# Kernel optimization log

Hardware: AMD Instinct MI355X
Metric: run time of the kernel (lower is better)

## Reference

```python
import jax, jax.numpy as jnp
import numpy as np

FILTS = 100  # conv padding = aconv_filts
SCALING = 2.0


def setup_inputs() -> dict:
    key = jax.random.key(0)
    ks = jax.random.split(key, 9)
    T, DUNITS, ATT, EPROJ, CH, K = 50000, 1024, 512, 512, 10, 2 * FILTS + 1
    return {
        "dec_z": jax.random.normal(ks[0], (1, DUNITS), jnp.float32),
        "att_prev": jax.random.uniform(ks[1], (1, T), jnp.float32),
        "pre_compute_enc_h": jax.random.normal(ks[2], (1, T, ATT), jnp.float32),
        "enc_h": jax.random.normal(ks[3], (1, T, EPROJ), jnp.float32),
        "mask": jnp.zeros((1, T), jnp.float32),
        "conv_w": jax.random.normal(ks[4], (CH, 1, K), jnp.float32) * 0.05,
        "w_att": jax.random.normal(ks[5], (ATT, CH), jnp.float32) * 0.05,
        "w_dec": jax.random.normal(ks[6], (ATT, DUNITS), jnp.float32) * 0.02,
        "w_gvec": jax.random.normal(ks[7], (1, ATT), jnp.float32) * 0.05,
        "b_gvec": jnp.zeros((1,), jnp.float32),
    }


def reference(dec_z, att_prev, pre_compute_enc_h, enc_h, mask, conv_w, w_att, w_dec, w_gvec, b_gvec):
    # loc_conv: 1-channel 1D conv over previous attention weights -> [1, CH, T]
    att_conv = jax.lax.conv_general_dilated(
        att_prev[:, None, :], conv_w, window_strides=(1,),
        padding=[(FILTS, FILTS)], dimension_numbers=("NCH", "OIH", "NCH"))
    # mlp_att: [1, T, ATT]
    att_conv = jnp.einsum("bct,ac->bta", att_conv, w_att)
    # mlp_dec, tiled over frames: [1, 1, ATT]
    dec_tiled = (dec_z @ w_dec.T)[:, None, :]
    # gvec(tanh(...)) -> scores e: [1, T]
    e = jnp.einsum("bta,a->bt", jnp.tanh(att_conv + pre_compute_enc_h + dec_tiled), w_gvec[0]) + b_gvec
    e = e + mask
    w = jax.nn.softmax(SCALING * e, axis=1)  # [1, T]
    c = jnp.sum(enc_h * w[..., None], axis=1)  # [1, EPROJ]
    return (c, w)
```

## Files before the change

### kernel.cpp

```cpp
#include <hip/hip_runtime.h>
#include <math.h>


constexpr int ATT    = 512;
constexpr int CH     = 10;
constexpr int PCH    = 12;
constexpr int KW     = 201;
constexpr int FILTS  = 100;
constexpr int DUNITS = 1024;
constexpr int NB1    = 1024;
constexpr int NB3    = 1024;
constexpr int CT     = 64;
constexpr float SCALING = 2.0f;

__device__ __forceinline__ float wave_reduce_sum(float v) {
    #pragma unroll
    for (int off = 32; off > 0; off >>= 1) v += __shfl_xor(v, off, 64);
    return v;
}

__device__ __forceinline__ float fast_tanh(float x) {
    float e = __expf(2.f * x);
    return 1.f - __fdividef(2.f, e + 1.f);
}

__global__ __launch_bounds__(256, 4) void k0_conv_dec(
    const float* __restrict__ att_prev,
    const float* __restrict__ conv_w,
    const float* __restrict__ dec_z,
    const float* __restrict__ w_dec,
    float* __restrict__ ws_aconv,
    float* __restrict__ ws_dec,
    float* __restrict__ out,
    int T, int nbconv)
{
    if ((int)blockIdx.x < nbconv) {
        __shared__ float s_ap[CT + KW - 1];
        __shared__ float s_wt[KW * 12];
        __shared__ float s_part[4 * CT * CH];
        const int t0 = blockIdx.x * CT;
        for (int i = threadIdx.x; i < CT + KW - 1; i += 256) {
            int t = t0 - FILTS + i;
            s_ap[i] = (t >= 0 && t < T) ? att_prev[t] : 0.f;
        }
        for (int i = threadIdx.x; i < CH * KW; i += 256) {
            int c = i % CH, k = i / CH;
            s_wt[k * 12 + c] = conv_w[c * KW + k];
        }
        __syncthreads();
        const int tl = threadIdx.x & 63;
        const int kq = threadIdx.x >> 6;
        float acc[CH];
        #pragma unroll
        for (int c = 0; c < CH; ++c) acc[c] = 0.f;
        for (int k = kq; k < KW; k += 4) {
            float x = s_ap[tl + k];
            const float4 w0 = *(const float4*)&s_wt[k * 12];
            const float4 w1 = *(const float4*)&s_wt[k * 12 + 4];
            const float2 w2 = *(const float2*)&s_wt[k * 12 + 8];
            acc[0] += x * w0.x; acc[1] += x * w0.y;
            acc[2] += x * w0.z; acc[3] += x * w0.w;
            acc[4] += x * w1.x; acc[5] += x * w1.y;
            acc[6] += x * w1.z; acc[7] += x * w1.w;
            acc[8] += x * w2.x; acc[9] += x * w2.y;
        }
        #pragma unroll
        for (int c = 0; c < CH; ++c) s_part[kq * (CT * CH) + tl * CH + c] = acc[c];
        __syncthreads();
        for (int idx = threadIdx.x; idx < CT * PCH; idx += 256) {
            int t = idx / PCH, c = idx % PCH;
            float v = 0.f;
            if (c < CH) {
                int j = t * CH + c;
                v = s_part[j] + s_part[CT * CH + j]
                  + s_part[2 * CT * CH + j] + s_part[3 * CT * CH + j];
            }
            if (t0 + t < T) ws_aconv[(size_t)(t0 + t) * PCH + c] = v;
        }
    } else {
        const int b    = blockIdx.x - nbconv;
        const int wid  = threadIdx.x >> 6;
        const int lane = threadIdx.x & 63;
        const int a    = b * 4 + wid;
        if (threadIdx.x < 4) out[b * 4 + threadIdx.x] = 0.f;
        const float4* wd = (const float4*)(w_dec + (size_t)a * DUNITS);
        const float4* dz = (const float4*)dec_z;
        float acc = 0.f;
        #pragma unroll
        for (int q = 0; q < 4; ++q) {
            float4 wv = wd[lane + q * 64];
            float4 zv = dz[lane + q * 64];
            acc += wv.x * zv.x + wv.y * zv.y + wv.z * zv.z + wv.w * zv.w;
        }
        acc = wave_reduce_sum(acc);
        if (lane == 0) ws_dec[a] = acc;
    }
}

__global__ __launch_bounds__(256, 2) void k1_scores(
    const float* __restrict__ pre,
    const float* __restrict__ mask,
    const float* __restrict__ w_att,
    const float* __restrict__ w_gvec,
    const float* __restrict__ b_gvec,
    const float* __restrict__ ws_dec,
    const float* __restrict__ ws_aconv,
    float* __restrict__ ws_e,
    float* __restrict__ ws_ms,
    int T)
{
    __shared__ float s_m[4], s_s[4];
    const int wid  = threadIdx.x >> 6;
    const int lane = threadIdx.x & 63;

    float wa[8][CH];
    #pragma unroll
    for (int j = 0; j < 4; ++j) {
        #pragma unroll
        for (int c = 0; c < CH; ++c) {
            wa[j][c]     = w_att[(lane * 4 + j) * CH + c];
            wa[4 + j][c] = w_att[(256 + lane * 4 + j) * CH + c];
        }
    }
    const float4 dlo = ((const float4*)ws_dec)[lane];
    const float4 dhi = ((const float4*)ws_dec)[64 + lane];
    const float4 glo = ((const float4*)w_gvec)[lane];
    const float4 ghi = ((const float4*)w_gvec)[64 + lane];
    const float  bg  = b_gvec[0];

    const float4* pre4 = (const float4*)pre;
    const float4* ac4  = (const float4*)ws_aconv;
    const int gw = blockIdx.x * 4 + wid;
    const int t0 = gw * 4;
    constexpr int S = NB1 * 16;

    float m = -INFINITY, s = 0.f;
    float4 pA0[4], pA1[4], pB0[4], pB1[4];
    float  mA[4], mB[4];
    float4 acx[4], acy[4], acz[4];

    auto loadp = [&](float4 (&P0)[4], float4 (&P1)[4], float (&MSK)[4], int tb) {
        #pragma unroll
        for (int i = 0; i < 4; ++i) {
            int t = tb + i;
            if (t < T) {
                P0[i]  = pre4[(size_t)t * 128 + lane];
                P1[i]  = pre4[(size_t)t * 128 + 64 + lane];
                MSK[i] = mask[t];
            }
        }
    };
    auto loada = [&](int tb) {
        #pragma unroll
        for (int i = 0; i < 4; ++i) {
            int t = tb + i;
            if (t < T) {
                acx[i] = ac4[(size_t)t * 3 + 0];
                acy[i] = ac4[(size_t)t * 3 + 1];
                acz[i] = ac4[(size_t)t * 3 + 2];
            }
        }
    };
    auto batch = [&](float4 (&P0)[4], float4 (&P1)[4], float (&MSK)[4], int tb,
                     float4 (&NP0)[4], float4 (&NP1)[4], float (&NM)[4], int tn,
                     bool pf) {
        if (pf) loadp(NP0, NP1, NM, tn);
        float y[4];
        #pragma unroll
        for (int i = 0; i < 4; ++i) {
            const int t = tb + i;
            y[i] = -INFINITY;
            if (t < T) {
                const float4 a0 = acx[i], a1 = acy[i], a2 = acz[i];
                float x0 = P0[i].x + dlo.x, x1 = P0[i].y + dlo.y;
                float x2 = P0[i].z + dlo.z, x3 = P0[i].w + dlo.w;
                float x4 = P1[i].x + dhi.x, x5 = P1[i].y + dhi.y;
                float x6 = P1[i].z + dhi.z, x7 = P1[i].w + dhi.w;
                #define AV(X, J) \
                    X += a0.x*wa[J][0] + a0.y*wa[J][1] + a0.z*wa[J][2] + a0.w*wa[J][3] \
                       + a1.x*wa[J][4] + a1.y*wa[J][5] + a1.z*wa[J][6] + a1.w*wa[J][7] \
                       + a2.x*wa[J][8] + a2.y*wa[J][9]
                AV(x0, 0); AV(x1, 1); AV(x2, 2); AV(x3, 3);
                AV(x4, 4); AV(x5, 5); AV(x6, 6); AV(x7, 7);
                #undef AV
                float acc = glo.x * fast_tanh(x0) + glo.y * fast_tanh(x1)
                          + glo.z * fast_tanh(x2) + glo.w * fast_tanh(x3)
                          + ghi.x * fast_tanh(x4) + ghi.y * fast_tanh(x5)
                          + ghi.z * fast_tanh(x6) + ghi.w * fast_tanh(x7);
                acc = wave_reduce_sum(acc);
                float yy = SCALING * (acc + bg + MSK[i]);
                if (lane == 0) ws_e[t] = yy;
                y[i] = yy;
            }
        }
        if (pf) loada(tn);
        float ymax = fmaxf(fmaxf(y[0], y[1]), fmaxf(y[2], y[3]));
        float nm = fmaxf(m, ymax);
        float add = __expf(y[0] - nm) + __expf(y[1] - nm)
                  + __expf(y[2] - nm) + __expf(y[3] - nm);
        s = s * __expf(m - nm) + add;
        m = nm;
    };

    loadp(pA0, pA1, mA, t0);
    loada(t0);
    batch(pA0, pA1, mA, t0,         pB0, pB1, mB, t0 + S,     true);
    batch(pB0, pB1, mB, t0 + S,     pA0, pA1, mA, t0 + 2 * S, true);
    batch(pA0, pA1, mA, t0 + 2 * S, pB0, pB1, mB, t0 + 3 * S, true);
    batch(pB0, pB1, mB, t0 + 3 * S, pA0, pA1, mA, 0,          false);

    if (lane == 0) { s_m[wid] = m; s_s[wid] = s; }
    __syncthreads();
    if (threadIdx.x == 0) {
        float M = s_m[0], Ssum = s_s[0];
        #pragma unroll
        for (int w = 1; w < 4; ++w) {
            float m2 = s_m[w], s2 = s_s[w];
            float nm = fmaxf(M, m2);
            Ssum = Ssum * __expf(M - nm) + s2 * __expf(m2 - nm);
            M = nm;
        }
        ws_ms[blockIdx.x * 2]     = M;
        ws_ms[blockIdx.x * 2 + 1] = Ssum;
    }
}

__global__ __launch_bounds__(256, 4) void k3_ctx(
    const float* __restrict__ enc_h,
    const float* __restrict__ ws_e,
    const float* __restrict__ ws_ms,
    float* __restrict__ out,
    int T)
{
    __shared__ float s_m[256], s_s[256];
    {
        float m = -INFINITY, s = 0.f;
        for (int i = threadIdx.x; i < NB1; i += 256) {
            float m2 = ws_ms[i * 2], s2 = ws_ms[i * 2 + 1];
            float nm = fmaxf(m, m2);
            s = s * __expf(m - nm) + s2 * __expf(m2 - nm);
            m = nm;
        }
        s_m[threadIdx.x] = m; s_s[threadIdx.x] = s;
        __syncthreads();
        for (int off = 128; off > 0; off >>= 1) {
            if ((int)threadIdx.x < off) {
                float M1 = s_m[threadIdx.x], S1 = s_s[threadIdx.x];
                float m2 = s_m[threadIdx.x + off], s2 = s_s[threadIdx.x + off];
                float nm = fmaxf(M1, m2);
                s_s[threadIdx.x] = S1 * __expf(M1 - nm) + s2 * __expf(m2 - nm);
                s_m[threadIdx.x] = nm;
            }
            __syncthreads();
        }
    }
    const float M  = s_m[0];
    const float IS = 1.f / s_s[0];

    const int wid  = threadIdx.x >> 6;
    const int lane = threadIdx.x & 63;
    const float4* eh4 = (const float4*)enc_h;
    const int gw = blockIdx.x * 4 + wid;
    const int t0 = gw * 4;
    constexpr int S = NB3 * 16;

    float4 a0 = make_float4(0.f, 0.f, 0.f, 0.f);
    float4 a1 = make_float4(0.f, 0.f, 0.f, 0.f);
    float4 eA0[4], eA1[4], eB0[4], eB1[4];
    float  yA[4], yB[4];

    auto loade = [&](float4 (&E0)[4], float4 (&E1)[4], float (&Y)[4], int tb) {
        #pragma unroll
        for (int i = 0; i < 4; ++i) {
            int t = tb + i;
            if (t < T) {
                E0[i] = eh4[(size_t)t * 128 + lane];
                E1[i] = eh4[(size_t)t * 128 + 64 + lane];
                Y[i]  = ws_e[t];
            }
        }
    };
    auto batch = [&](float4 (&E0)[4], float4 (&E1)[4], float (&Y)[4], int tb,
                     float4 (&NE0)[4], float4 (&NE1)[4], float (&NY)[4], int tn,
                     bool pf) {
        if (pf) loade(NE0, NE1, NY, tn);
        #pragma unroll
        for (int i = 0; i < 4; ++i) {
            int t = tb + i;
            if (t < T) {
                float w = __expf(Y[i] - M) * IS;
                if (lane == 0) out[ATT + t] = w;
                a0.x += w * E0[i].x; a0.y += w * E0[i].y;
                a0.z += w * E0[i].z; a0.w += w * E0[i].w;
                a1.x += w * E1[i].x; a1.y += w * E1[i].y;
                a1.z += w * E1[i].z; a1.w += w * E1[i].w;
            }
        }
    };

    loade(eA0, eA1, yA, t0);
    batch(eA0, eA1, yA, t0,         eB0, eB1, yB, t0 + S,     true);
    batch(eB0, eB1, yB, t0 + S,     eA0, eA1, yA, t0 + 2 * S, true);
    batch(eA0, eA1, yA, t0 + 2 * S, eB0, eB1, yB, t0 + 3 * S, true);
    batch(eB0, eB1, yB, t0 + 3 * S, eA0, eA1, yA, 0,          false);

    __syncthreads();
    __shared__ float4 s_c[4 * 128];
    s_c[wid * 128 + lane]      = a0;
    s_c[wid * 128 + 64 + lane] = a1;
    __syncthreads();
    const float* sc = (const float*)s_c;
    for (int a = threadIdx.x; a < ATT; a += 256) {
        float v = sc[a] + sc[512 + a] + sc[1024 + a] + sc[1536 + a];
        atomicAdd(&out[a], v);
    }
}

extern "C" void kernel_launch(void* const* d_in, const int* in_sizes, int n_in,
                              void* d_out, int out_size, void* d_ws, size_t ws_size,
                              hipStream_t stream)
{
    const float* dec_z    = (const float*)d_in[0];
    const float* att_prev = (const float*)d_in[1];
    const float* pre      = (const float*)d_in[2];
    const float* enc_h    = (const float*)d_in[3];
    const float* mask     = (const float*)d_in[4];
    const float* conv_w   = (const float*)d_in[5];
    const float* w_att    = (const float*)d_in[6];
    const float* w_dec    = (const float*)d_in[7];
    const float* w_gvec   = (const float*)d_in[8];
    const float* b_gvec   = (const float*)d_in[9];
    const int T = in_sizes[1];

    float* ws       = (float*)d_ws;
    float* ws_dec   = ws;
    float* ws_aconv = ws_dec + ATT;
    float* ws_e     = ws_aconv + (size_t)T * PCH;
    float* ws_ms    = ws_e + T;
    float* out      = (float*)d_out;

    const int nbconv = (T + CT - 1) / CT;

    hipLaunchKernelGGL(k0_conv_dec, dim3(nbconv + ATT / 4), dim3(256), 0, stream,
                       att_prev, conv_w, dec_z, w_dec, ws_aconv, ws_dec, out, T, nbconv);
    hipLaunchKernelGGL(k1_scores, dim3(NB1), dim3(256), 0, stream,
                       pre, mask, w_att, w_gvec, b_gvec, ws_dec, ws_aconv,
                       ws_e, ws_ms, T);
    hipLaunchKernelGGL(k3_ctx, dim3(NB3), dim3(256), 0, stream,
                       enc_h, ws_e, ws_ms, out, T);
}
```

Measured before the change: 299.0 us.

## Fuse context accumulation into score kernel with online-softmax rescaling

```diff
diff --git a/kernel.cpp b/kernel.cpp
--- a/kernel.cpp
+++ b/kernel.cpp
@@ -9,7 +9,6 @@
 constexpr int FILTS  = 100;
 constexpr int DUNITS = 1024;
 constexpr int NB1    = 1024;
-constexpr int NB3    = 1024;
 constexpr int CT     = 64;
 constexpr float SCALING = 2.0f;
 
@@ -31,7 +30,6 @@
     const float* __restrict__ w_dec,
     float* __restrict__ ws_aconv,
     float* __restrict__ ws_dec,
-    float* __restrict__ out,
     int T, int nbconv)
 {
     if ((int)blockIdx.x < nbconv) {
@@ -82,7 +80,6 @@
         const int wid  = threadIdx.x >> 6;
         const int lane = threadIdx.x & 63;
         const int a    = b * 4 + wid;
-        if (threadIdx.x < 4) out[b * 4 + threadIdx.x] = 0.f;
         const float4* wd = (const float4*)(w_dec + (size_t)a * DUNITS);
         const float4* dz = (const float4*)dec_z;
         float acc = 0.f;
@@ -97,8 +94,9 @@
     }
 }
 
-__global__ __launch_bounds__(256, 2) void k1_scores(
+__global__ __launch_bounds__(256, 3) void k1_scores(
     const float* __restrict__ pre,
+    const float* __restrict__ enc_h,
     const float* __restrict__ mask,
     const float* __restrict__ w_att,
     const float* __restrict__ w_gvec,
@@ -107,9 +105,9 @@
     const float* __restrict__ ws_aconv,
     float* __restrict__ ws_e,
     float* __restrict__ ws_ms,
+    float* __restrict__ ws_c,
     int T)
 {
-    __shared__ float s_m[4], s_s[4];
     const int wid  = threadIdx.x >> 6;
     const int lane = threadIdx.x & 63;
 
@@ -129,12 +127,15 @@
     const float  bg  = b_gvec[0];
 
     const float4* pre4 = (const float4*)pre;
+    const float4* eh4  = (const float4*)enc_h;
     const float4* ac4  = (const float4*)ws_aconv;
     const int gw = blockIdx.x * 4 + wid;
     const int t0 = gw * 4;
     constexpr int S = NB1 * 16;
 
     float m = -INFINITY, s = 0.f;
+    float4 cA0 = make_float4(0.f, 0.f, 0.f, 0.f);
+    float4 cA1 = make_float4(0.f, 0.f, 0.f, 0.f);
     float4 pA0[4], pA1[4], pB0[4], pB1[4];
     float  mA[4], mB[4];
     float4 acx[4], acy[4], acz[4];
@@ -165,6 +166,17 @@
                      float4 (&NP0)[4], float4 (&NP1)[4], float (&NM)[4], int tn,
                      bool pf) {
         if (pf) loadp(NP0, NP1, NM, tn);
+        float4 E0[4], E1[4];
+        const float4 z4 = make_float4(0.f, 0.f, 0.f, 0.f);
+        #pragma unroll
+        for (int i = 0; i < 4; ++i) {
+            int t = tb + i;
+            E0[i] = z4; E1[i] = z4;
+            if (t < T) {
+                E0[i] = eh4[(size_t)t * 128 + lane];
+                E1[i] = eh4[(size_t)t * 128 + 64 + lane];
+            }
+        }
         float y[4];
         #pragma unroll
         for (int i = 0; i < 4; ++i) {
@@ -196,9 +208,18 @@
         if (pf) loada(tn);
         float ymax = fmaxf(fmaxf(y[0], y[1]), fmaxf(y[2], y[3]));
         float nm = fmaxf(m, ymax);
-        float add = __expf(y[0] - nm) + __expf(y[1] - nm)
-                  + __expf(y[2] - nm) + __expf(y[3] - nm);
-        s = s * __expf(m - nm) + add;
+        float sc = __expf(m - nm);
+        float w0 = __expf(y[0] - nm), w1 = __expf(y[1] - nm);
+        float w2 = __expf(y[2] - nm), w3 = __expf(y[3] - nm);
+        s = s * sc + (w0 + w1 + w2 + w3);
+        cA0.x = cA0.x * sc + w0*E0[0].x + w1*E0[1].x + w2*E0[2].x + w3*E0[3].x;
+        cA0.y = cA0.y * sc + w0*E0[0].y + w1*E0[1].y + w2*E0[2].y + w3*E0[3].y;
+        cA0.z = cA0.z * sc + w0*E0[0].z + w1*E0[1].z + w2*E0[2].z + w3*E0[3].z;
+        cA0.w = cA0.w * sc + w0*E0[0].w + w1*E0[1].w + w2*E0[2].w + w3*E0[3].w;
+        cA1.x = cA1.x * sc + w0*E1[0].x + w1*E1[1].x + w2*E1[2].x + w3*E1[3].x;
+        cA1.y = cA1.y * sc + w0*E1[0].y + w1*E1[1].y + w2*E1[2].y + w3*E1[3].y;
+        cA1.z = cA1.z * sc + w0*E1[0].z + w1*E1[1].z + w2*E1[2].z + w3*E1[3].z;
+        cA1.w = cA1.w * sc + w0*E1[0].w + w1*E1[1].w + w2*E1[2].w + w3*E1[3].w;
         m = nm;
     };
 
@@ -209,26 +230,32 @@
     batch(pA0, pA1, mA, t0 + 2 * S, pB0, pB1, mB, t0 + 3 * S, true);
     batch(pB0, pB1, mB, t0 + 3 * S, pA0, pA1, mA, 0,          false);
 
-    if (lane == 0) { s_m[wid] = m; s_s[wid] = s; }
+    __shared__ float4 s_c[4 * 128];
+    __shared__ float  s_mw[4], s_sw[4];
+    s_c[wid * 128 + lane]      = cA0;
+    s_c[wid * 128 + 64 + lane] = cA1;
+    if (lane == 0) { s_mw[wid] = m; s_sw[wid] = s; }
     __syncthreads();
+    const float mb = fmaxf(fmaxf(s_mw[0], s_mw[1]), fmaxf(s_mw[2], s_mw[3]));
+    const float sc0 = __expf(s_mw[0] - mb), sc1 = __expf(s_mw[1] - mb);
+    const float sc2 = __expf(s_mw[2] - mb), sc3 = __expf(s_mw[3] - mb);
+    const float* scf = (const float*)s_c;
+    for (int a = threadIdx.x; a < ATT; a += 256) {
+        float v = sc0 * scf[a] + sc1 * scf[512 + a]
+                + sc2 * scf[1024 + a] + sc3 * scf[1536 + a];
+        ws_c[(size_t)blockIdx.x * ATT + a] = v;
+    }
     if (threadIdx.x == 0) {
-        float M = s_m[0], Ssum = s_s[0];
-        #pragma unroll
-        for (int w = 1; w < 4; ++w) {
-            float m2 = s_m[w], s2 = s_s[w];
-            float nm = fmaxf(M, m2);
-            Ssum = Ssum * __expf(M - nm) + s2 * __expf(m2 - nm);
-            M = nm;
-        }
-        ws_ms[blockIdx.x * 2]     = M;
-        ws_ms[blockIdx.x * 2 + 1] = Ssum;
-    }
-}
-
-__global__ __launch_bounds__(256, 4) void k3_ctx(
-    const float* __restrict__ enc_h,
+        ws_ms[blockIdx.x * 2]     = mb;
+        ws_ms[blockIdx.x * 2 + 1] = sc0 * s_sw[0] + sc1 * s_sw[1]
+                                  + sc2 * s_sw[2] + sc3 * s_sw[3];
+    }
+}
+
+__global__ __launch_bounds__(256, 4) void k2_final(
     const float* __restrict__ ws_e,
     const float* __restrict__ ws_ms,
+    const float* __restrict__ ws_c,
     float* __restrict__ out,
     int T)
 {
@@ -257,63 +284,30 @@
     const float M  = s_m[0];
     const float IS = 1.f / s_s[0];
 
-    const int wid  = threadIdx.x >> 6;
-    const int lane = threadIdx.x & 63;
-    const float4* eh4 = (const float4*)enc_h;
-    const int gw = blockIdx.x * 4 + wid;
-    const int t0 = gw * 4;
-    constexpr int S = NB3 * 16;
-
-    float4 a0 = make_float4(0.f, 0.f, 0.f, 0.f);
-    float4 a1 = make_float4(0.f, 0.f, 0.f, 0.f);
-    float4 eA0[4], eA1[4], eB0[4], eB1[4];
-    float  yA[4], yB[4];
-
-    auto loade = [&](float4 (&E0)[4], float4 (&E1)[4], float (&Y)[4], int tb) {
-        #pragma unroll
-        for (int i = 0; i < 4; ++i) {
-            int t = tb + i;
-            if (t < T) {
-                E0[i] = eh4[(size_t)t * 128 + lane];
-                E1[i] = eh4[(size_t)t * 128 + 64 + lane];
-                Y[i]  = ws_e[t];
-            }
-        }
-    };
-    auto batch = [&](float4 (&E0)[4], float4 (&E1)[4], float (&Y)[4], int tb,
-                     float4 (&NE0)[4], float4 (&NE1)[4], float (&NY)[4], int tn,
-                     bool pf) {
-        if (pf) loade(NE0, NE1, NY, tn);
-        #pragma unroll
-        for (int i = 0; i < 4; ++i) {
-            int t = tb + i;
-            if (t < T) {
-                float w = __expf(Y[i] - M) * IS;
-                if (lane == 0) out[ATT + t] = w;
-                a0.x += w * E0[i].x; a0.y += w * E0[i].y;
-                a0.z += w * E0[i].z; a0.w += w * E0[i].w;
-                a1.x += w * E1[i].x; a1.y += w * E1[i].y;
-                a1.z += w * E1[i].z; a1.w += w * E1[i].w;
-            }
-        }
-    };
-
-    loade(eA0, eA1, yA, t0);
-    batch(eA0, eA1, yA, t0,         eB0, eB1, yB, t0 + S,     true);
-    batch(eB0, eB1, yB, t0 + S,     eA0, eA1, yA, t0 + 2 * S, true);
-    batch(eA0, eA1, yA, t0 + 2 * S, eB0, eB1, yB, t0 + 3 * S, true);
-    batch(eB0, eB1, yB, t0 + 3 * S, eA0, eA1, yA, 0,          false);
-
-    __syncthreads();
-    __shared__ float4 s_c[4 * 128];
-    s_c[wid * 128 + lane]      = a0;
-    s_c[wid * 128 + 64 + lane] = a1;
-    __syncthreads();
-    const float* sc = (const float*)s_c;
-    for (int a = threadIdx.x; a < ATT; a += 256) {
-        float v = sc[a] + sc[512 + a] + sc[1024 + a] + sc[1536 + a];
-        atomicAdd(&out[a], v);
-    }
+    if (blockIdx.x < 32) {
+        __shared__ float s_scale[NB1];
+        for (int b = threadIdx.x; b < NB1; b += 256)
+            s_scale[b] = __expf(ws_ms[b * 2] - M);
+        __syncthreads();
+        const int al = threadIdx.x >> 4;
+        const int ch = threadIdx.x & 15;
+        const int a  = blockIdx.x * 16 + al;
+        float acc = 0.f;
+        for (int b = ch * (NB1 / 16); b < (ch + 1) * (NB1 / 16); ++b)
+            acc += s_scale[b] * ws_c[(size_t)b * ATT + a];
+        __shared__ float s_p[256];
+        s_p[threadIdx.x] = acc;
+        __syncthreads();
+        if (ch == 0) {
+            float v = 0.f;
+            #pragma unroll
+            for (int k = 0; k < 16; ++k) v += s_p[al * 16 + k];
+            out[a] = v * IS;
+        }
+    }
+
+    const int t = blockIdx.x * 256 + threadIdx.x;
+    if (t < T) out[ATT + t] = __expf(ws_e[t] - M) * IS;
 }
 
 extern "C" void kernel_launch(void* const* d_in, const int* in_sizes, int n_in,
@@ -337,15 +331,17 @@
     float* ws_aconv = ws_dec + ATT;
     float* ws_e     = ws_aconv + (size_t)T * PCH;
     float* ws_ms    = ws_e + T;
+    float* ws_c     = ws_ms + NB1 * 2;
     float* out      = (float*)d_out;
 
     const int nbconv = (T + CT - 1) / CT;
+    const int nb2    = (T + 255) / 256;
 
     hipLaunchKernelGGL(k0_conv_dec, dim3(nbconv + ATT / 4), dim3(256), 0, stream,
-                       att_prev, conv_w, dec_z, w_dec, ws_aconv, ws_dec, out, T, nbconv);
+                       att_prev, conv_w, dec_z, w_dec, ws_aconv, ws_dec, T, nbconv);
     hipLaunchKernelGGL(k1_scores, dim3(NB1), dim3(256), 0, stream,
-                       pre, mask, w_att, w_gvec, b_gvec, ws_dec, ws_aconv,
-                       ws_e, ws_ms, T);
-    hipLaunchKernelGGL(k3_ctx, dim3(NB3), dim3(256), 0, stream,
-                       enc_h, ws_e, ws_ms, out, T);
-}
+                       pre, enc_h, mask, w_att, w_gvec, b_gvec, ws_dec, ws_aconv,
+                       ws_e, ws_ms, ws_c, T);
+    hipLaunchKernelGGL(k2_final, dim3(nb2), dim3(256), 0, stream,
+                       ws_e, ws_ms, ws_c, out, T);
+}
```

Result: slower. 475.8 us (+59.1%).
